# Kernel optimization log

Measured on AMD Instinct MI355X. Metric: run time of the kernel, lower is better.

Reference implementation:

```python
import jax, jax.numpy as jnp
import numpy as np

EPS = 1e-5

def layer_norm(x, gamma, beta):
    mu = jnp.mean(x, axis=-1, keepdims=True)
    var = jnp.var(x, axis=-1, keepdims=True)
    return (x - mu) * jax.lax.rsqrt(var + EPS) * gamma + beta

def setup_inputs() -> dict:
    key = jax.random.key(0)
    ks = jax.random.split(key, 4)
    B, L, D = 32, 4096, 768
    x = jax.random.normal(ks[0], (B, L, D), dtype=jnp.float32)
    w_kv = jax.random.normal(ks[1], (2 * D, D), dtype=jnp.float32) * (D ** -0.5)
    query = jax.random.normal(ks[2], (D,), dtype=jnp.float32)
    gamma1 = jnp.ones((D,), jnp.float32)
    beta1 = jnp.zeros((D,), jnp.float32)
    gamma2 = jnp.ones((D,), jnp.float32)
    beta2 = jnp.zeros((D,), jnp.float32)
    return {"x": x, "w_kv": w_kv, "query": query,
            "gamma1": gamma1, "beta1": beta1,
            "gamma2": gamma2, "beta2": beta2}

def reference(x, w_kv, query, gamma1, beta1, gamma2, beta2):
    B, L, D = x.shape
    H = 8
    Dh = D // H
    scale = Dh ** -0.5
    xn = layer_norm(x, gamma1, beta1)                      # [B,L,D]
    kv = jnp.einsum('bld,ed->ble', xn, w_kv)               # [B,L,2D]
    k, v = jnp.split(kv, 2, axis=-1)                       # [B,L,D] each
    k = k.reshape(B, L, H, Dh)                             # [B,L,H,Dh]
    v = v.reshape(B, L, H, Dh)
    q = query.reshape(H, Dh)                               # [H,Dh]
    dots = jnp.einsum('hd,blhd->bhl', q, k) * scale        # [B,H,L]
    attn = jax.nn.softmax(dots, axis=-1)                   # [B,H,L]
    out = jnp.einsum('bhl,blhd->bhd', attn, v)             # [B,H,Dh]
    out = out.reshape(B, D)                                # [B,D]
    return layer_norm(out, gamma2, beta2)
```

## Files before the change

kernel.cpp:

```cpp
#include <hip/hip_runtime.h>
#include <stdint.h>

#define DD 768
#define HN 8
#define LL 4096
#define BB 32
#define ROWS 64
#define NBLK (BB * LL / ROWS)
#define DEPTH 4
#define PSTR 772

#define GLOBAL_AS __attribute__((address_space(1)))
#define LDS_AS    __attribute__((address_space(3)))

#define DPP_STEP(x, ctrl, rmask, bc)                                           \
  x += __int_as_float(__builtin_amdgcn_update_dpp(                             \
      0, __float_as_int(x), (ctrl), (rmask), 0xf, (bc)))

__device__ __forceinline__ void wave_sum4(float& a, float& b, float& c, float& d) {
  DPP_STEP(a, 0x111, 0xf, true);  DPP_STEP(b, 0x111, 0xf, true);
  DPP_STEP(c, 0x111, 0xf, true);  DPP_STEP(d, 0x111, 0xf, true);
  DPP_STEP(a, 0x112, 0xf, true);  DPP_STEP(b, 0x112, 0xf, true);
  DPP_STEP(c, 0x112, 0xf, true);  DPP_STEP(d, 0x112, 0xf, true);
  DPP_STEP(a, 0x114, 0xf, true);  DPP_STEP(b, 0x114, 0xf, true);
  DPP_STEP(c, 0x114, 0xf, true);  DPP_STEP(d, 0x114, 0xf, true);
  DPP_STEP(a, 0x118, 0xf, true);  DPP_STEP(b, 0x118, 0xf, true);
  DPP_STEP(c, 0x118, 0xf, true);  DPP_STEP(d, 0x118, 0xf, true);
  DPP_STEP(a, 0x142, 0xa, false); DPP_STEP(b, 0x142, 0xa, false);
  DPP_STEP(c, 0x142, 0xa, false); DPP_STEP(d, 0x142, 0xa, false);
  DPP_STEP(a, 0x143, 0xc, false); DPP_STEP(b, 0x143, 0xc, false);
  DPP_STEP(c, 0x143, 0xc, false); DPP_STEP(d, 0x143, 0xc, false);
  a = __int_as_float(__builtin_amdgcn_readlane(__float_as_int(a), 63));
  b = __int_as_float(__builtin_amdgcn_readlane(__float_as_int(b), 63));
  c = __int_as_float(__builtin_amdgcn_readlane(__float_as_int(c), 63));
  d = __int_as_float(__builtin_amdgcn_readlane(__float_as_int(d), 63));
}

__device__ __forceinline__ void wave_sum2(float& a, float& b) {
  DPP_STEP(a, 0x111, 0xf, true);  DPP_STEP(b, 0x111, 0xf, true);
  DPP_STEP(a, 0x112, 0xf, true);  DPP_STEP(b, 0x112, 0xf, true);
  DPP_STEP(a, 0x114, 0xf, true);  DPP_STEP(b, 0x114, 0xf, true);
  DPP_STEP(a, 0x118, 0xf, true);  DPP_STEP(b, 0x118, 0xf, true);
  DPP_STEP(a, 0x142, 0xa, false); DPP_STEP(b, 0x142, 0xa, false);
  DPP_STEP(a, 0x143, 0xc, false); DPP_STEP(b, 0x143, 0xc, false);
  a = __int_as_float(__builtin_amdgcn_readlane(__float_as_int(a), 63));
  b = __int_as_float(__builtin_amdgcn_readlane(__float_as_int(b), 63));
}

__global__ __launch_bounds__(768) void k_qk(const float* __restrict__ wkv,
                                            const float* __restrict__ query,
                                            const float* __restrict__ gamma1,
                                            float* __restrict__ qk) {
  int h = blockIdx.x;
  int d = threadIdx.x;
  const float* wbase = wkv + (size_t)h * 96 * DD + d;
  const float* qb = query + h * 96;
  float acc = 0.f;
  #pragma unroll 8
  for (int i = 0; i < 96; ++i) acc = fmaf(qb[i], wbase[(size_t)i * DD], acc);
  acc *= 0.10206207261596577f * gamma1[d];
  __shared__ float wsum[12];
  __shared__ float meanv;
  float v = acc;
  #pragma unroll
  for (int off = 1; off < 64; off <<= 1) v += __shfl_xor(v, off, 64);
  if ((d & 63) == 0) wsum[d >> 6] = v;
  __syncthreads();
  if (d == 0) {
    float s = 0.f;
    #pragma unroll
    for (int i = 0; i < 12; ++i) s += wsum[i];
    meanv = s * (1.f / 768.f);
  }
  __syncthreads();
  qk[h * DD + d] = acc - meanv;
}

__global__ __launch_bounds__(64, 2) void k_main(
    const float* __restrict__ x, const float* __restrict__ qk,
    float* __restrict__ part) {
  const int lane = threadIdx.x;
  __shared__ float lds[DEPTH][DD];

  float4 q[HN][3];
  #pragma unroll
  for (int h = 0; h < HN; ++h)
    #pragma unroll
    for (int j = 0; j < 3; ++j)
      q[h][j] = *reinterpret_cast<const float4*>(qk + h * DD + j * 256 + lane * 4);
  asm volatile("s_waitcnt vmcnt(0)" ::: "memory");

  float4 S[HN][3];
  float se[HN], ch[HN];
  #pragma unroll
  for (int h = 0; h < HN; ++h) {
    se[h] = 0.f; ch[h] = 0.f;
    #pragma unroll
    for (int j = 0; j < 3; ++j) S[h][j] = make_float4(0.f, 0.f, 0.f, 0.f);
  }

  const float* gbase = x + (size_t)blockIdx.x * ROWS * DD;

  #define STAGE(R)                                                             \
    {                                                                          \
      const float* gt = gbase + (size_t)(R) * DD;                              \
      float* db = &lds[(R) & (DEPTH - 1)][0];                                  \
      _Pragma("unroll")                                                        \
      for (int i = 0; i < 3; ++i)                                              \
        __builtin_amdgcn_global_load_lds(                                      \
            (const GLOBAL_AS uint32_t*)(gt + i * 256 + lane * 4),              \
            (LDS_AS uint32_t*)(db + i * 256), 16, 0, 0);                       \
    }

  #define COMPUTE(RR)                                                          \
    {                                                                          \
      const float* row = &lds[(RR) & (DEPTH - 1)][0];                          \
      float4 c0 = *reinterpret_cast<const float4*>(row + lane * 4);            \
      float4 c1 = *reinterpret_cast<const float4*>(row + 256 + lane * 4);      \
      float4 c2 = *reinterpret_cast<const float4*>(row + 512 + lane * 4);      \
      float s1 = 0.f, s2 = 0.f;                                                \
      float dt[HN];                                                            \
      _Pragma("unroll") for (int h = 0; h < HN; ++h) dt[h] = 0.f;              \
      ACC4(c0, 0) ACC4(c1, 1) ACC4(c2, 2)                                      \
      wave_sum4(s1, s2, dt[0], dt[1]);                                         \
      wave_sum4(dt[2], dt[3], dt[4], dt[5]);                                   \
      wave_sum2(dt[6], dt[7]);                                                 \
      float mu   = s1 * (1.f / 768.f);                                         \
      float var  = fmaf(-mu, mu, s2 * (1.f / 768.f));                          \
      float rstd = rsqrtf(var + 1e-5f);                                        \
      float sh   = -mu * rstd;                                                 \
      float pe   = rstd * 1.44269504f;                                         \
      _Pragma("unroll")                                                        \
      for (int h = 0; h < HN; ++h) {                                           \
        float p = exp2f(dt[h] * pe);                                           \
        se[h] += p;                                                            \
        ch[h] = fmaf(p, sh, ch[h]);                                            \
        float a = p * rstd;                                                    \
        S[h][0].x = fmaf(a, c0.x, S[h][0].x);                                  \
        S[h][0].y = fmaf(a, c0.y, S[h][0].y);                                  \
        S[h][0].z = fmaf(a, c0.z, S[h][0].z);                                  \
        S[h][0].w = fmaf(a, c0.w, S[h][0].w);                                  \
        S[h][1].x = fmaf(a, c1.x, S[h][1].x);                                  \
        S[h][1].y = fmaf(a, c1.y, S[h][1].y);                                  \
        S[h][1].z = fmaf(a, c1.z, S[h][1].z);                                  \
        S[h][1].w = fmaf(a, c1.w, S[h][1].w);                                  \
        S[h][2].x = fmaf(a, c2.x, S[h][2].x);                                  \
        S[h][2].y = fmaf(a, c2.y, S[h][2].y);                                  \
        S[h][2].z = fmaf(a, c2.z, S[h][2].z);                                  \
        S[h][2].w = fmaf(a, c2.w, S[h][2].w);                                  \
      }                                                                        \
    }

#define ACC4(cv, J)                                                            \
      s1 += cv.x + cv.y + cv.z + cv.w;                                         \
      s2 = fmaf(cv.x, cv.x, s2); s2 = fmaf(cv.y, cv.y, s2);                    \
      s2 = fmaf(cv.z, cv.z, s2); s2 = fmaf(cv.w, cv.w, s2);                    \
      _Pragma("unroll")                                                        \
      for (int h = 0; h < HN; ++h) {                                           \
        dt[h] = fmaf(cv.x, q[h][J].x, dt[h]);                                  \
        dt[h] = fmaf(cv.y, q[h][J].y, dt[h]);                                  \
        dt[h] = fmaf(cv.z, q[h][J].z, dt[h]);                                  \
        dt[h] = fmaf(cv.w, q[h][J].w, dt[h]);                                  \
      }

  STAGE(0) STAGE(1) STAGE(2)

  #pragma unroll 1
  for (int r = 0; r <= ROWS - 4; ++r) {
    STAGE(r + 3)
    asm volatile("s_waitcnt vmcnt(9)" ::: "memory");
    COMPUTE(r)
  }
  asm volatile("s_waitcnt vmcnt(6)" ::: "memory");
  COMPUTE(ROWS - 3)
  asm volatile("s_waitcnt vmcnt(3)" ::: "memory");
  COMPUTE(ROWS - 2)
  asm volatile("s_waitcnt vmcnt(0)" ::: "memory");
  COMPUTE(ROWS - 1)

  #undef ACC4
  #undef COMPUTE
  #undef STAGE

  float* pb = part + (size_t)blockIdx.x * (HN * PSTR);
  #pragma unroll
  for (int h = 0; h < HN; ++h) {
    #pragma unroll
    for (int j = 0; j < 3; ++j) {
      float4 v = S[h][j];
      v.x += ch[h]; v.y += ch[h]; v.z += ch[h]; v.w += ch[h];
      *reinterpret_cast<float4*>(pb + h * PSTR + j * 256 + lane * 4) = v;
    }
  }
  if (lane == 0) {
    #pragma unroll
    for (int h = 0; h < HN; ++h) pb[h * PSTR + 768] = se[h];
  }
}

__global__ __launch_bounds__(256) void k_red(const float* __restrict__ part,
                                             const float* __restrict__ gamma1,
                                             const float* __restrict__ beta1,
                                             float* __restrict__ xbar) {
  int b = blockIdx.x >> 3;
  int h = blockIdx.x & 7;
  int t = threadIdx.x;
  const int CPB = LL / ROWS;
  const float* pb = part + ((size_t)b * CPB * HN + h) * PSTR;
  float se = 0.f, a0 = 0.f, a1 = 0.f, a2 = 0.f;
  for (int i = 0; i < CPB; ++i) {
    const float* P = pb + (size_t)i * HN * PSTR;
    se += P[768];
    a0 += P[t];
    a1 += P[t + 256];
    a2 += P[t + 512];
  }
  float inv = 1.f / se;
  size_t ob = ((size_t)b * HN + h) * DD;
  xbar[ob + t]       = fmaf(gamma1[t],       a0 * inv, beta1[t]);
  xbar[ob + t + 256] = fmaf(gamma1[t + 256], a1 * inv, beta1[t + 256]);
  xbar[ob + t + 512] = fmaf(gamma1[t + 512], a2 * inv, beta1[t + 512]);
}

__global__ __launch_bounds__(256) void k_proj(
    const float* __restrict__ xbar, const float* __restrict__ wkv,
    float* __restrict__ outp) {
  int b  = blockIdx.x / 3;
  int gc = blockIdx.x % 3;
  int t  = threadIdx.x;
  __shared__ float xb[HN * DD];
  #pragma unroll
  for (int k = 0; k < 24; ++k) xb[k * 256 + t] = xbar[(size_t)b * HN * DD + k * 256 + t];
  __syncthreads();

  int g = gc * 256 + t;
  int h = g / 96;
  const float4* wrow = reinterpret_cast<const float4*>(wkv + (size_t)(DD + g) * DD);
  const float* xh = xb + h * DD;
  float acc = 0.f;
  #pragma unroll 4
  for (int e = 0; e < 192; ++e) {
    float4 w = wrow[e];
    acc = fmaf(w.x, xh[e * 4 + 0], acc);
    acc = fmaf(w.y, xh[e * 4 + 1], acc);
    acc = fmaf(w.z, xh[e * 4 + 2], acc);
    acc = fmaf(w.w, xh[e * 4 + 3], acc);
  }
  outp[(size_t)b * DD + g] = acc;
}

__global__ __launch_bounds__(768) void k_ln2(
    const float* __restrict__ outp, const float* __restrict__ gamma2,
    const float* __restrict__ beta2, float* __restrict__ out) {
  int b = blockIdx.x;
  int t = threadIdx.x;
  __shared__ float rs1[12], rs2[12];
  __shared__ float smu, srstd;
  float o = outp[(size_t)b * DD + t];
  float v1 = o, v2 = o * o;
  #pragma unroll
  for (int off = 1; off < 64; off <<= 1) {
    v1 += __shfl_xor(v1, off, 64);
    v2 += __shfl_xor(v2, off, 64);
  }
  int wv = t >> 6, ln = t & 63;
  if (ln == 0) { rs1[wv] = v1; rs2[wv] = v2; }
  __syncthreads();
  if (t == 0) {
    float s1 = 0.f, s2 = 0.f;
    #pragma unroll
    for (int w = 0; w < 12; ++w) { s1 += rs1[w]; s2 += rs2[w]; }
    float mu = s1 * (1.f / 768.f);
    float var = fmaf(-mu, mu, s2 * (1.f / 768.f));
    smu = mu;
    srstd = rsqrtf(var + 1e-5f);
  }
  __syncthreads();
  out[(size_t)b * DD + t] = fmaf((o - smu) * srstd, gamma2[t], beta2[t]);
}

extern "C" void kernel_launch(void* const* d_in, const int* in_sizes, int n_in,
                              void* d_out, int out_size, void* d_ws, size_t ws_size,
                              hipStream_t stream) {
  const float* x     = (const float*)d_in[0];
  const float* wkv   = (const float*)d_in[1];
  const float* query = (const float*)d_in[2];
  const float* g1    = (const float*)d_in[3];
  const float* b1    = (const float*)d_in[4];
  const float* g2    = (const float*)d_in[5];
  const float* b2    = (const float*)d_in[6];
  float* out = (float*)d_out;
  float* ws  = (float*)d_ws;

  float* qk   = ws;
  float* part = ws + 8192;
  float* xbar = part + (size_t)NBLK * HN * PSTR;
  float* outp = xbar + (size_t)BB * HN * DD;

  k_qk  <<<HN,      768, 0, stream>>>(wkv, query, g1, qk);
  k_main<<<NBLK,    64,  0, stream>>>(x, qk, part);
  k_red <<<BB * HN, 256, 0, stream>>>(part, g1, b1, xbar);
  k_proj<<<BB * 3,  256, 0, stream>>>(xbar, wkv, outp);
  k_ln2 <<<BB,      768, 0, stream>>>(outp, g2, b2, out);
}
```

Before: 181.3 us.

## Split heads across two waves per block to cut per-wave register pressure

k_main now runs two waves per block, each handling four of the eight heads over the same rows with its own LDS ring buffer. This halves the per-wave accumulator and query registers, allowing more waves in flight to hide latency. In exchange, each row of x is loaded twice (relying on cache for reuse) and the layer-norm statistics and row loads are duplicated per wave.

```diff
diff --git a/kernel.cpp b/kernel.cpp
--- a/kernel.cpp
+++ b/kernel.cpp
@@ -76,24 +76,28 @@
   qk[h * DD + d] = acc - meanv;
 }
 
-__global__ __launch_bounds__(64, 2) void k_main(
+__global__ __launch_bounds__(128, 3) void k_main(
     const float* __restrict__ x, const float* __restrict__ qk,
     float* __restrict__ part) {
-  const int lane = threadIdx.x;
-  __shared__ float lds[DEPTH][DD];
-
-  float4 q[HN][3];
-  #pragma unroll
-  for (int h = 0; h < HN; ++h)
+  const int lane = threadIdx.x & 63;
+  const int wave = threadIdx.x >> 6;
+  const int h0 = wave * 4;
+
+  __shared__ float lds[2][DEPTH][DD];
+  float* ring = &lds[wave][0][0];
+
+  float4 q[4][3];
+  #pragma unroll
+  for (int h = 0; h < 4; ++h)
     #pragma unroll
     for (int j = 0; j < 3; ++j)
-      q[h][j] = *reinterpret_cast<const float4*>(qk + h * DD + j * 256 + lane * 4);
+      q[h][j] = *reinterpret_cast<const float4*>(qk + (h0 + h) * DD + j * 256 + lane * 4);
   asm volatile("s_waitcnt vmcnt(0)" ::: "memory");
 
-  float4 S[HN][3];
-  float se[HN], ch[HN];
-  #pragma unroll
-  for (int h = 0; h < HN; ++h) {
+  float4 S[4][3];
+  float se[4], ch[4];
+  #pragma unroll
+  for (int h = 0; h < 4; ++h) {
     se[h] = 0.f; ch[h] = 0.f;
     #pragma unroll
     for (int j = 0; j < 3; ++j) S[h][j] = make_float4(0.f, 0.f, 0.f, 0.f);
@@ -104,7 +108,7 @@
   #define STAGE(R)                                                             \
     {                                                                          \
       const float* gt = gbase + (size_t)(R) * DD;                              \
-      float* db = &lds[(R) & (DEPTH - 1)][0];                                  \
+      float* db = ring + ((R) & (DEPTH - 1)) * DD;                             \
       _Pragma("unroll")                                                        \
       for (int i = 0; i < 3; ++i)                                              \
         __builtin_amdgcn_global_load_lds(                                      \
@@ -114,24 +118,22 @@
 
   #define COMPUTE(RR)                                                          \
     {                                                                          \
-      const float* row = &lds[(RR) & (DEPTH - 1)][0];                          \
+      const float* row = ring + ((RR) & (DEPTH - 1)) * DD;                     \
       float4 c0 = *reinterpret_cast<const float4*>(row + lane * 4);            \
       float4 c1 = *reinterpret_cast<const float4*>(row + 256 + lane * 4);      \
       float4 c2 = *reinterpret_cast<const float4*>(row + 512 + lane * 4);      \
       float s1 = 0.f, s2 = 0.f;                                                \
-      float dt[HN];                                                            \
-      _Pragma("unroll") for (int h = 0; h < HN; ++h) dt[h] = 0.f;              \
+      float dt[4] = {0.f, 0.f, 0.f, 0.f};                                      \
       ACC4(c0, 0) ACC4(c1, 1) ACC4(c2, 2)                                      \
       wave_sum4(s1, s2, dt[0], dt[1]);                                         \
-      wave_sum4(dt[2], dt[3], dt[4], dt[5]);                                   \
-      wave_sum2(dt[6], dt[7]);                                                 \
+      wave_sum2(dt[2], dt[3]);                                                 \
       float mu   = s1 * (1.f / 768.f);                                         \
       float var  = fmaf(-mu, mu, s2 * (1.f / 768.f));                          \
       float rstd = rsqrtf(var + 1e-5f);                                        \
       float sh   = -mu * rstd;                                                 \
       float pe   = rstd * 1.44269504f;                                         \
       _Pragma("unroll")                                                        \
-      for (int h = 0; h < HN; ++h) {                                           \
+      for (int h = 0; h < 4; ++h) {                                            \
         float p = exp2f(dt[h] * pe);                                           \
         se[h] += p;                                                            \
         ch[h] = fmaf(p, sh, ch[h]);                                            \
@@ -156,7 +158,7 @@
       s2 = fmaf(cv.x, cv.x, s2); s2 = fmaf(cv.y, cv.y, s2);                    \
       s2 = fmaf(cv.z, cv.z, s2); s2 = fmaf(cv.w, cv.w, s2);                    \
       _Pragma("unroll")                                                        \
-      for (int h = 0; h < HN; ++h) {                                           \
+      for (int h = 0; h < 4; ++h) {                                            \
         dt[h] = fmaf(cv.x, q[h][J].x, dt[h]);                                  \
         dt[h] = fmaf(cv.y, q[h][J].y, dt[h]);                                  \
         dt[h] = fmaf(cv.z, q[h][J].z, dt[h]);                                  \
@@ -182,9 +184,9 @@
   #undef COMPUTE
   #undef STAGE
 
-  float* pb = part + (size_t)blockIdx.x * (HN * PSTR);
-  #pragma unroll
-  for (int h = 0; h < HN; ++h) {
+  float* pb = part + (size_t)blockIdx.x * (HN * PSTR) + (size_t)h0 * PSTR;
+  #pragma unroll
+  for (int h = 0; h < 4; ++h) {
     #pragma unroll
     for (int j = 0; j < 3; ++j) {
       float4 v = S[h][j];
@@ -194,7 +196,7 @@
   }
   if (lane == 0) {
     #pragma unroll
-    for (int h = 0; h < HN; ++h) pb[h * PSTR + 768] = se[h];
+    for (int h = 0; h < 4; ++h) pb[h * PSTR + 768] = se[h];
   }
 }
 
@@ -298,7 +300,7 @@
   float* outp = xbar + (size_t)BB * HN * DD;
 
   k_qk  <<<HN,      768, 0, stream>>>(wkv, query, g1, qk);
-  k_main<<<NBLK,    64,  0, stream>>>(x, qk, part);
+  k_main<<<NBLK,    128, 0, stream>>>(x, qk, part);
   k_red <<<BB * HN, 256, 0, stream>>>(part, g1, b1, xbar);
   k_proj<<<BB * 3,  256, 0, stream>>>(xbar, wkv, outp);
   k_ln2 <<<BB,      768, 0, stream>>>(outp, g2, b2, out);
```

New measurement: 215.3 us. 1.19x slower.

## Deepen LDS row ring to six slots and move qk mean-centering into main kernel

Applied to the files above, without the earlier changes.

Raises the global-to-LDS prefetch ring from 4 to 6 rows with explicit slot counters and adjusted vmcnt waits, so more row loads are in flight per wave. The qk kernel is split into 24 blocks of 256 threads and no longer does a block reduction. Each k_main block instead recomputes the per-head mean of the query-key vector with a wave reduction and subtracts it from its registers. The k_red loop is also unrolled. The trade-off is more LDS per block (which may reduce occupancy) and some redundant mean computation in every main block.

```diff
diff --git a/kernel.cpp b/kernel.cpp
--- a/kernel.cpp
+++ b/kernel.cpp
@@ -7,7 +7,7 @@
 #define BB 32
 #define ROWS 64
 #define NBLK (BB * LL / ROWS)
-#define DEPTH 4
+#define DEPTH 6
 #define PSTR 772
 
 #define GLOBAL_AS __attribute__((address_space(1)))
@@ -47,48 +47,56 @@
   b = __int_as_float(__builtin_amdgcn_readlane(__float_as_int(b), 63));
 }
 
-__global__ __launch_bounds__(768) void k_qk(const float* __restrict__ wkv,
+__global__ __launch_bounds__(256) void k_qk(const float* __restrict__ wkv,
                                             const float* __restrict__ query,
                                             const float* __restrict__ gamma1,
-                                            float* __restrict__ qk) {
-  int h = blockIdx.x;
-  int d = threadIdx.x;
+                                            float* __restrict__ qkraw) {
+  int h = blockIdx.x / 3;
+  int d = (blockIdx.x % 3) * 256 + threadIdx.x;
   const float* wbase = wkv + (size_t)h * 96 * DD + d;
   const float* qb = query + h * 96;
   float acc = 0.f;
   #pragma unroll 8
   for (int i = 0; i < 96; ++i) acc = fmaf(qb[i], wbase[(size_t)i * DD], acc);
-  acc *= 0.10206207261596577f * gamma1[d];
-  __shared__ float wsum[12];
-  __shared__ float meanv;
-  float v = acc;
-  #pragma unroll
-  for (int off = 1; off < 64; off <<= 1) v += __shfl_xor(v, off, 64);
-  if ((d & 63) == 0) wsum[d >> 6] = v;
-  __syncthreads();
-  if (d == 0) {
-    float s = 0.f;
-    #pragma unroll
-    for (int i = 0; i < 12; ++i) s += wsum[i];
-    meanv = s * (1.f / 768.f);
-  }
-  __syncthreads();
-  qk[h * DD + d] = acc - meanv;
+  qkraw[h * DD + d] = acc * 0.10206207261596577f * gamma1[d];
 }
 
 __global__ __launch_bounds__(64, 2) void k_main(
-    const float* __restrict__ x, const float* __restrict__ qk,
+    const float* __restrict__ x, const float* __restrict__ qkraw,
     float* __restrict__ part) {
   const int lane = threadIdx.x;
   __shared__ float lds[DEPTH][DD];
+  float* ring = &lds[0][0];
 
   float4 q[HN][3];
   #pragma unroll
   for (int h = 0; h < HN; ++h)
     #pragma unroll
     for (int j = 0; j < 3; ++j)
-      q[h][j] = *reinterpret_cast<const float4*>(qk + h * DD + j * 256 + lane * 4);
+      q[h][j] = *reinterpret_cast<const float4*>(qkraw + h * DD + j * 256 + lane * 4);
   asm volatile("s_waitcnt vmcnt(0)" ::: "memory");
+
+  {
+    float m[HN];
+    #pragma unroll
+    for (int h = 0; h < HN; ++h) {
+      float s = 0.f;
+      #pragma unroll
+      for (int j = 0; j < 3; ++j)
+        s += q[h][j].x + q[h][j].y + q[h][j].z + q[h][j].w;
+      m[h] = s;
+    }
+    wave_sum4(m[0], m[1], m[2], m[3]);
+    wave_sum4(m[4], m[5], m[6], m[7]);
+    #pragma unroll
+    for (int h = 0; h < HN; ++h) {
+      float mv = m[h] * (1.f / 768.f);
+      #pragma unroll
+      for (int j = 0; j < 3; ++j) {
+        q[h][j].x -= mv; q[h][j].y -= mv; q[h][j].z -= mv; q[h][j].w -= mv;
+      }
+    }
+  }
 
   float4 S[HN][3];
   float se[HN], ch[HN];
@@ -101,10 +109,10 @@
 
   const float* gbase = x + (size_t)blockIdx.x * ROWS * DD;
 
-  #define STAGE(R)                                                             \
+  #define STAGE(R, SLOT)                                                       \
     {                                                                          \
       const float* gt = gbase + (size_t)(R) * DD;                              \
-      float* db = &lds[(R) & (DEPTH - 1)][0];                                  \
+      float* db = ring + (SLOT) * DD;                                          \
       _Pragma("unroll")                                                        \
       for (int i = 0; i < 3; ++i)                                              \
         __builtin_amdgcn_global_load_lds(                                      \
@@ -112,9 +120,9 @@
             (LDS_AS uint32_t*)(db + i * 256), 16, 0, 0);                       \
     }
 
-  #define COMPUTE(RR)                                                          \
+  #define COMPUTE(SLOT)                                                        \
     {                                                                          \
-      const float* row = &lds[(RR) & (DEPTH - 1)][0];                          \
+      const float* row = ring + (SLOT) * DD;                                   \
       float4 c0 = *reinterpret_cast<const float4*>(row + lane * 4);            \
       float4 c1 = *reinterpret_cast<const float4*>(row + 256 + lane * 4);      \
       float4 c2 = *reinterpret_cast<const float4*>(row + 512 + lane * 4);      \
@@ -163,20 +171,27 @@
         dt[h] = fmaf(cv.w, q[h][J].w, dt[h]);                                  \
       }
 
-  STAGE(0) STAGE(1) STAGE(2)
-
+  STAGE(0, 0) STAGE(1, 1) STAGE(2, 2) STAGE(3, 3) STAGE(4, 4)
+
+  int sIn = 5, sCur = 0;
   #pragma unroll 1
-  for (int r = 0; r <= ROWS - 4; ++r) {
-    STAGE(r + 3)
-    asm volatile("s_waitcnt vmcnt(9)" ::: "memory");
-    COMPUTE(r)
-  }
+  for (int r = 0; r <= ROWS - 6; ++r) {
+    STAGE(r + 5, sIn)
+    sIn = (sIn == DEPTH - 1) ? 0 : sIn + 1;
+    asm volatile("s_waitcnt vmcnt(15)" ::: "memory");
+    COMPUTE(sCur)
+    sCur = (sCur == DEPTH - 1) ? 0 : sCur + 1;
+  }
+  asm volatile("s_waitcnt vmcnt(12)" ::: "memory");
+  COMPUTE(sCur) sCur = (sCur == DEPTH - 1) ? 0 : sCur + 1;
+  asm volatile("s_waitcnt vmcnt(9)" ::: "memory");
+  COMPUTE(sCur) sCur = (sCur == DEPTH - 1) ? 0 : sCur + 1;
   asm volatile("s_waitcnt vmcnt(6)" ::: "memory");
-  COMPUTE(ROWS - 3)
+  COMPUTE(sCur) sCur = (sCur == DEPTH - 1) ? 0 : sCur + 1;
   asm volatile("s_waitcnt vmcnt(3)" ::: "memory");
-  COMPUTE(ROWS - 2)
+  COMPUTE(sCur) sCur = (sCur == DEPTH - 1) ? 0 : sCur + 1;
   asm volatile("s_waitcnt vmcnt(0)" ::: "memory");
-  COMPUTE(ROWS - 1)
+  COMPUTE(sCur)
 
   #undef ACC4
   #undef COMPUTE
@@ -208,6 +223,7 @@
   const int CPB = LL / ROWS;
   const float* pb = part + ((size_t)b * CPB * HN + h) * PSTR;
   float se = 0.f, a0 = 0.f, a1 = 0.f, a2 = 0.f;
+  #pragma unroll 4
   for (int i = 0; i < CPB; ++i) {
     const float* P = pb + (size_t)i * HN * PSTR;
     se += P[768];
@@ -292,13 +308,13 @@
   float* out = (float*)d_out;
   float* ws  = (float*)d_ws;
 
-  float* qk   = ws;
-  float* part = ws + 8192;
-  float* xbar = part + (size_t)NBLK * HN * PSTR;
-  float* outp = xbar + (size_t)BB * HN * DD;
-
-  k_qk  <<<HN,      768, 0, stream>>>(wkv, query, g1, qk);
-  k_main<<<NBLK,    64,  0, stream>>>(x, qk, part);
+  float* qkraw = ws;
+  float* part  = ws + 8192;
+  float* xbar  = part + (size_t)NBLK * HN * PSTR;
+  float* outp  = xbar + (size_t)BB * HN * DD;
+
+  k_qk  <<<24,      256, 0, stream>>>(wkv, query, g1, qkraw);
+  k_main<<<NBLK,    64,  0, stream>>>(x, qkraw, part);
   k_red <<<BB * HN, 256, 0, stream>>>(part, g1, b1, xbar);
   k_proj<<<BB * 3,  256, 0, stream>>>(xbar, wkv, outp);
   k_ln2 <<<BB,      768, 0, stream>>>(outp, g2, b2, out);
```

New measurement: 188.6 us. 1.04x slower.
